# Performance work log

Hardware: AMD Instinct MI355X
Metric: run time of the kernel (lower is better)

The kernel has to match this reference:

```python
import jax, jax.numpy as jnp
import numpy as np

EPS = 1e-5
NUM_HEADS = 8

def _ln(x, g, b):
    mu = jnp.mean(x, axis=-1, keepdims=True)
    var = jnp.mean(jnp.square(x - mu), axis=-1, keepdims=True)
    return (x - mu) * jax.lax.rsqrt(var + EPS) * g + b

def setup_inputs() -> dict:
    key = jax.random.key(0)
    ks = jax.random.split(key, 20)
    B, S, N, D, F = 16, 12, 325, 256, 2048
    sd = 0.02
    return {
        "x": jax.random.normal(ks[0], (B, S, N, D), jnp.float32),
        "Wq": jax.random.normal(ks[1], (D, D), jnp.float32) * sd,
        "bq": jax.random.normal(ks[2], (D,), jnp.float32) * sd,
        "Wk": jax.random.normal(ks[3], (D, D), jnp.float32) * sd,
        "bk": jax.random.normal(ks[4], (D,), jnp.float32) * sd,
        "Wv": jax.random.normal(ks[5], (D, D), jnp.float32) * sd,
        "bv": jax.random.normal(ks[6], (D,), jnp.float32) * sd,
        "Wo": jax.random.normal(ks[7], (D, D), jnp.float32) * sd,
        "bo": jax.random.normal(ks[8], (D,), jnp.float32) * sd,
        "W1": jax.random.normal(ks[9], (D, F), jnp.float32) * sd,
        "b1": jax.random.normal(ks[10], (F,), jnp.float32) * sd,
        "W2": jax.random.normal(ks[11], (F, D), jnp.float32) * sd,
        "b2": jax.random.normal(ks[12], (D,), jnp.float32) * sd,
        "g1": jax.random.uniform(ks[13], (D,), jnp.float32, 0.5, 1.5),
        "beta1": jax.random.normal(ks[14], (D,), jnp.float32) * sd,
        "g2": jax.random.uniform(ks[15], (D,), jnp.float32, 0.5, 1.5),
        "beta2": jax.random.normal(ks[16], (D,), jnp.float32) * sd,
        "dim": -2,
    }

def reference(x, Wq, bq, Wk, bk, Wv, bv, Wo, bo, W1, b1, W2, b2, g1, beta1, g2, beta2, dim):
    # transpose attention dim to -2 (identity when dim == -2)
    x = jnp.swapaxes(x, dim, -2)
    B, S, N, D = x.shape
    H = NUM_HEADS
    hd = D // H
    residual = x
    # QKV projections
    q = (x @ Wq + bq).reshape(B, S, N, H, hd)
    k = (x @ Wk + bk).reshape(B, S, N, H, hd)
    v = (x @ Wv + bv).reshape(B, S, N, H, hd)
    # attention over node dim (axis -2), per head; scale by sqrt(head_dim)
    scores = jnp.einsum('bsnhd,bsmhd->bshnm', q, k) / jnp.sqrt(jnp.float32(hd))
    attn = jax.nn.softmax(scores, axis=-1)
    out = jnp.einsum('bshnm,bsmhd->bsnhd', attn, v).reshape(B, S, N, D)
    out = out @ Wo + bo
    # dropout is identity (p=0); residual + LN
    out = _ln(residual + out, g1, beta1)
    residual = out
    ff = jax.nn.relu(out @ W1 + b1) @ W2 + b2
    out = _ln(residual + ff, g2, beta2)
    return jnp.swapaxes(out, dim, -2)
```

## Files before the change

kernel.cpp:

```cpp
#include <hip/hip_runtime.h>

typedef unsigned short ushortT;
typedef unsigned short us4 __attribute__((ext_vector_type(4)));
typedef short s4 __attribute__((ext_vector_type(4)));
typedef short s8 __attribute__((ext_vector_type(8)));
typedef float f4 __attribute__((ext_vector_type(4)));

__device__ __forceinline__ float bf2f(ushortT u) {
  union { unsigned u; float f; } x; x.u = ((unsigned)u) << 16; return x.f;
}
__device__ __forceinline__ ushortT f2bf(float f) {
  union { float f; unsigned u; } x; x.f = f;
  unsigned r = x.u + 0x7fffu + ((x.u >> 16) & 1u);
  return (ushortT)(r >> 16);
}
__device__ __forceinline__ ushortT bftrunc(float f) {
  union { float f; unsigned u; } x; x.f = f;
  return (ushortT)(x.u >> 16);
}
__device__ __forceinline__ s4 lo4(s8 v) { return __builtin_shufflevector(v, v, 0, 1, 2, 3); }
__device__ __forceinline__ s4 hi4(s8 v) { return __builtin_shufflevector(v, v, 4, 5, 6, 7); }
__device__ __forceinline__ s8 cat(s4 a, s4 b) { return __builtin_shufflevector(a, b, 0, 1, 2, 3, 4, 5, 6, 7); }

__device__ __forceinline__ void gld16(const ushortT* g, ushortT* l) {
  __builtin_amdgcn_global_load_lds(
      (const __attribute__((address_space(1))) void*)g,
      (__attribute__((address_space(3))) void*)l, 16, 0, 0);
}

#define CONV_BLOCKS 15600
__global__ void prep(const float* __restrict__ x,
                     const float* __restrict__ Wq, const float* __restrict__ Wk,
                     const float* __restrict__ Wv, const float* __restrict__ Wo,
                     const float* __restrict__ W1, const float* __restrict__ W2,
                     const float* __restrict__ bq, const float* __restrict__ bk,
                     const float* __restrict__ bv,
                     ushortT* __restrict__ xb, ushortT* __restrict__ WqkvT,
                     ushortT* __restrict__ WoT, ushortT* __restrict__ W1T,
                     ushortT* __restrict__ W2P, float* __restrict__ bqkv)
{
  if (blockIdx.x < CONV_BLOCKS) {
    size_t base = ((size_t)blockIdx.x * 256 + threadIdx.x) * 4;
    f4 v = *(const f4*)(x + base);
    us4 o; o[0]=f2bf(v[0]); o[1]=f2bf(v[1]); o[2]=f2bf(v[2]); o[3]=f2bf(v[3]);
    *(us4*)(xb + base) = o;
    return;
  }
  long e = (long)(blockIdx.x - CONV_BLOCKS) * 256 + threadIdx.x;
  if (e < 196608) {
    int seg = e >> 16; int p = e & 65535; int r = p >> 8, c = p & 255;
    const float* W = seg == 0 ? Wq : (seg == 1 ? Wk : Wv);
    WqkvT[(size_t)(seg * 256 + c) * 256 + r] = f2bf(W[p]);
  } else if (e < 262144) {
    int p = e - 196608; int r = p >> 8, c = p & 255;
    WoT[(size_t)c * 256 + r] = f2bf(Wo[p]);
  } else if (e < 786432) {
    int p = e - 262144; int r = p >> 11, c = p & 2047;
    W1T[(size_t)c * 256 + r] = f2bf(W1[p]);
  } else if (e < 1310720) {
    int p = e - 786432; int r = p >> 8, c = p & 255;
    int rp = (r & ~63) | ((r & 15) << 2) | ((r >> 4) & 3);
    W2P[(size_t)c * 2048 + rp] = f2bf(W2[p]);
  } else {
    int p = (int)(e - 1310720);
    const float* b = (p >> 8) == 0 ? bq : ((p >> 8) == 1 ? bv : bv);
    b = (p >> 8) == 0 ? bq : ((p >> 8) == 1 ? bk : bv);
    bqkv[p] = b[p & 255];
  }
}
#define PREP_BLOCKS (CONV_BLOCKS + 5123)

#define BM 128
#define BN 128
#define BK 32

template <typename CT>
__global__ __launch_bounds__(256, 4) void gemm_async(
    const ushortT* __restrict__ A, const ushortT* __restrict__ Bt,
    const float* __restrict__ bias,
    CT* __restrict__ O0, CT* __restrict__ O1, CT* __restrict__ O2,
    int M, int N, int K, int relu, int route, float s0)
{
  __shared__ ushortT As[BM * BK];
  __shared__ ushortT Bs[BN * BK];
  const int tileN = blockIdx.x * BN;
  const int tileM = blockIdx.y * BM;
  const int tid  = threadIdx.x;
  const int wave = tid >> 6, lane = tid & 63;
  const int wm = (wave >> 1) * 64, wn = (wave & 1) * 64;
  const int lrow = lane & 15;
  const int kq = (lane >> 4) * 8;

  const int srow = wave * 16 + (lane >> 2);
  const int scol = (lane & 3) * 8;
  int ar0 = tileM + srow;        if (ar0 > M - 1) ar0 = M - 1;
  int ar1 = tileM + 64 + srow;   if (ar1 > M - 1) ar1 = M - 1;
  const ushortT* ap0 = A + (size_t)ar0 * K + scol;
  const ushortT* ap1 = A + (size_t)ar1 * K + scol;
  const ushortT* bp0 = Bt + (size_t)(tileN + srow) * K + scol;
  const ushortT* bp1 = Bt + (size_t)(tileN + 64 + srow) * K + scol;
  ushortT* asd0 = As + wave * 512;
  ushortT* asd1 = As + 2048 + wave * 512;
  ushortT* bsd0 = Bs + wave * 512;
  ushortT* bsd1 = Bs + 2048 + wave * 512;

  f4 acc[4][4];
#pragma unroll
  for (int i = 0; i < 4; i++)
#pragma unroll
    for (int j = 0; j < 4; j++) acc[i][j] = 0.f;

  for (int k0 = 0; k0 < K; k0 += BK) {
    gld16(ap0, asd0); gld16(ap1, asd1);
    gld16(bp0, bsd0); gld16(bp1, bsd1);
    ap0 += BK; ap1 += BK; bp0 += BK; bp1 += BK;
    __syncthreads();
    s8 af[4], bfr[4];
#pragma unroll
    for (int mi = 0; mi < 4; mi++)
      af[mi] = *(const s8*)(As + (wm + mi * 16 + lrow) * BK + kq);
#pragma unroll
    for (int ni = 0; ni < 4; ni++)
      bfr[ni] = *(const s8*)(Bs + (wn + ni * 16 + lrow) * BK + kq);
#pragma unroll
    for (int mi = 0; mi < 4; mi++)
#pragma unroll
      for (int ni = 0; ni < 4; ni++)
        acc[mi][ni] = __builtin_amdgcn_mfma_f32_16x16x32_bf16(af[mi], bfr[ni], acc[mi][ni], 0, 0, 0);
    __syncthreads();
  }

  CT* dst; int col0, ostride;
  float oscale = 1.f;
  if (route) {
    int seg = tileN >> 8;
    dst = seg == 0 ? O0 : (seg == 1 ? O1 : O2);
    col0 = tileN & 255; ostride = 256;
    if (seg == 0) oscale = s0;
  } else {
    dst = O0; col0 = tileN; ostride = N;
  }
  const int crow0 = (lane >> 4) * 4;
  const int ccol  = lane & 15;
#pragma unroll
  for (int mi = 0; mi < 4; mi++) {
#pragma unroll
    for (int ni = 0; ni < 4; ni++) {
      int lcol = wn + ni * 16 + ccol;
      float bvv = bias[tileN + lcol];
#pragma unroll
      for (int r = 0; r < 4; r++) {
        int grow = tileM + wm + mi * 16 + crow0 + r;
        if (grow < M) {
          float v = (acc[mi][ni][r] + bvv) * oscale;
          if (relu) v = fmaxf(v, 0.f);
          if constexpr (sizeof(CT) == 2)
            dst[(size_t)grow * ostride + col0 + lcol] = f2bf(v);
          else
            dst[(size_t)grow * ostride + col0 + lcol] = v;
        }
      }
    }
  }
}

#define NQ 325
#define NPAD 384
#define KSTR 36
#define VSTR 388
#define PSTR 72

__global__ __launch_bounds__(256, 2) void attn_mfma(
    const ushortT* __restrict__ q, const ushortT* __restrict__ k,
    const ushortT* __restrict__ v, ushortT* __restrict__ out)
{
  __shared__ ushortT ks[NPAD * KSTR];
  __shared__ ushortT vt[32 * VSTR];
  __shared__ ushortT ps[4 * 16 * PSTR];
  const int bs = blockIdx.x >> 3;
  const int h  = blockIdx.x & 7;
  const size_t rowbase = (size_t)bs * NQ;
  const int hcol = h * 32;
  const int tid = threadIdx.x;
  const int wave = tid >> 6, lane = tid & 63;
  const int g = lane >> 4;
  const int c = lane & 15;

  for (int idx = tid; idx < NPAD * 4; idx += 256) {
    int row = idx >> 2, part = idx & 3;
    s8 kv = 0, vv = 0;
    if (row < NQ) {
      kv = *(const s8*)(k + (rowbase + row) * 256 + hcol + part * 8);
      vv = *(const s8*)(v + (rowbase + row) * 256 + hcol + part * 8);
    }
    *(s4*)(ks + row * KSTR + part * 8)     = lo4(kv);
    *(s4*)(ks + row * KSTR + part * 8 + 4) = hi4(kv);
    int pcol = (row & ~63) | ((row & 15) << 2) | ((row >> 4) & 3);
#pragma unroll
    for (int j = 0; j < 8; j++)
      vt[(part * 8 + j) * VSTR + pcol] = (ushortT)vv[j];
  }
  __syncthreads();

  s8 ones;
#pragma unroll
  for (int j = 0; j < 8; j++) ones[j] = (short)0x3F80;

  ushortT* psw = ps + wave * 16 * PSTR;

  for (int strip = wave; strip < 21; strip += 4) {
    const int m0 = strip * 16;
    s8 qf = 0;
    {
      int qrow = m0 + c;
      if (qrow < NQ) qf = *(const s8*)(q + (rowbase + qrow) * 256 + hcol + g * 8);
    }
    f4 ov0 = 0.f, ov1 = 0.f, ovs = 0.f;

    for (int ch = 0; ch < 6; ++ch) {
      const int nbase = ch * 64;
      f4 sc[4];
#pragma unroll
      for (int t = 0; t < 4; ++t) {
        const ushortT* kr = ks + (nbase + t * 16 + c) * KSTR + g * 8;
        s8 kf = cat(*(const s4*)kr, *(const s4*)(kr + 4));
        f4 z = 0.f;
        sc[t] = __builtin_amdgcn_mfma_f32_16x16x32_bf16(qf, kf, z, 0, 0, 0);
      }
#pragma unroll
      for (int t = 0; t < 4; ++t)
#pragma unroll
        for (int r = 0; r < 4; ++r)
          sc[t][r] = __expf(sc[t][r]);
      if (ch == 5) {
#pragma unroll
        for (int t = 0; t < 4; ++t) {
          bool valid = (t == 0) && (c < 5);
#pragma unroll
          for (int r = 0; r < 4; ++r)
            if (!valid) sc[t][r] = 0.f;
        }
      }
#pragma unroll
      for (int r = 0; r < 4; ++r) {
        us4 pw;
#pragma unroll
        for (int t = 0; t < 4; ++t) pw[t] = bftrunc(sc[t][r]);
        *(us4*)(psw + (g * 4 + r) * PSTR + c * 4) = pw;
      }
#pragma unroll
      for (int kt = 0; kt < 2; ++kt) {
        s8 pf = *(const s8*)(psw + c * PSTR + kt * 32 + g * 8);
        ovs = __builtin_amdgcn_mfma_f32_16x16x32_bf16(pf, ones, ovs, 0, 0, 0);
        const ushortT* vr0 = vt + c * VSTR + nbase + kt * 32 + g * 8;
        const ushortT* vr1 = vt + (16 + c) * VSTR + nbase + kt * 32 + g * 8;
        s8 vf0 = cat(*(const s4*)vr0, *(const s4*)(vr0 + 4));
        s8 vf1 = cat(*(const s4*)vr1, *(const s4*)(vr1 + 4));
        ov0 = __builtin_amdgcn_mfma_f32_16x16x32_bf16(pf, vf0, ov0, 0, 0, 0);
        ov1 = __builtin_amdgcn_mfma_f32_16x16x32_bf16(pf, vf1, ov1, 0, 0, 0);
      }
    }
#pragma unroll
    for (int r = 0; r < 4; ++r) {
      int gm = m0 + g * 4 + r;
      if (gm < NQ) {
        float inv = 1.f / ovs[r];
        out[(rowbase + gm) * 256 + hcol + c]      = f2bf(ov0[r] * inv);
        out[(rowbase + gm) * 256 + hcol + 16 + c] = f2bf(ov1[r] * inv);
      }
    }
  }
}

#define HSTR2 72

__global__ __launch_bounds__(512, 2) void ffn_fused(
    const ushortT* __restrict__ y, const ushortT* __restrict__ W1T,
    const float* __restrict__ b1, const ushortT* __restrict__ W2P,
    const float* __restrict__ b2, float* __restrict__ outp, int M)
{
  __shared__ ushortT w1c[2][64 * 256];
  __shared__ ushortT w2c[2][256 * 64];
  __shared__ ushortT hs[128 * HSTR2];
  __shared__ ushortT b1l[2048];

  const int tid = threadIdx.x;
  const int w = tid >> 6, lane = tid & 63;
  const int g = lane >> 4, c = lane & 15;
  const int mq = w >> 1, nh = w & 1;
  const int Mtile = blockIdx.x * 128;

  {
    f4 bv = *(const f4*)(b1 + tid * 4);
    us4 o; o[0]=f2bf(bv[0]); o[1]=f2bf(bv[1]); o[2]=f2bf(bv[2]); o[3]=f2bf(bv[3]);
    *(us4*)(b1l + tid * 4) = o;
  }

#pragma unroll
  for (int i = 0; i < 4; ++i) {
    int qq = tid * 8 + i * 4096;
    int r1 = qq >> 8;
    int c1 = (qq & 255) ^ ((r1 & 7) << 3);
    gld16(W1T + (size_t)r1 * 256 + c1, w1c[0] + w * 512 + i * 4096);
    int r2 = qq >> 6;
    int c2 = (qq & 63) ^ ((r2 & 7) << 3);
    gld16(W2P + (size_t)r2 * 2048 + c2, w2c[0] + w * 512 + i * 4096);
  }

  int yrow = Mtile + w * 16 + c; if (yrow > M - 1) yrow = M - 1;
  const ushortT* yp = y + (size_t)yrow * 256 + g * 8;
  s8 yv[8];
#pragma unroll
  for (int ksi = 0; ksi < 8; ++ksi) yv[ksi] = *(const s8*)(yp + ksi * 32);

  float b2v[8];
#pragma unroll
  for (int nt = 0; nt < 8; ++nt) b2v[nt] = b2[nh * 128 + nt * 16 + c];

  f4 acc[2][8];
#pragma unroll
  for (int mt = 0; mt < 2; ++mt)
#pragma unroll
    for (int nt = 0; nt < 8; ++nt) acc[mt][nt] = 0.f;

  __syncthreads();

  for (int chn = 0; chn < 32; ++chn) {
    const int b = chn & 1;
    const ushortT* w1b = w1c[b];
    const ushortT* w2b = w2c[b];

    if (chn + 1 < 32) {
      const size_t f1 = (size_t)(chn + 1) * 64 * 256;
      const int k1 = (chn + 1) * 64;
#pragma unroll
      for (int i = 0; i < 4; ++i) {
        int qq = tid * 8 + i * 4096;
        int r1 = qq >> 8;
        int c1 = (qq & 255) ^ ((r1 & 7) << 3);
        gld16(W1T + f1 + (size_t)r1 * 256 + c1, w1c[b ^ 1] + w * 512 + i * 4096);
        int r2 = qq >> 6;
        int c2 = (qq & 63) ^ ((r2 & 7) << 3);
        gld16(W2P + (size_t)r2 * 2048 + k1 + c2, w2c[b ^ 1] + w * 512 + i * 4096);
      }
    }

    f4 sc[4];
#pragma unroll
    for (int t = 0; t < 4; ++t) sc[t] = 0.f;
#pragma unroll
    for (int ksi = 0; ksi < 8; ++ksi) {
#pragma unroll
      for (int t = 0; t < 4; ++t) {
        int f = t * 16 + c;
        s8 wf = *(const s8*)(w1b + f * 256 + ((ksi * 32 + g * 8) ^ ((f & 7) << 3)));
        sc[t] = __builtin_amdgcn_mfma_f32_16x16x32_bf16(yv[ksi], wf, sc[t], 0, 0, 0);
      }
    }
#pragma unroll
    for (int t = 0; t < 4; ++t) {
      float bv = bf2f(b1l[chn * 64 + t * 16 + c]);
#pragma unroll
      for (int r = 0; r < 4; ++r) sc[t][r] = fmaxf(sc[t][r] + bv, 0.f);
    }
#pragma unroll
    for (int r = 0; r < 4; ++r) {
      us4 pw;
#pragma unroll
      for (int t = 0; t < 4; ++t) pw[t] = f2bf(sc[t][r]);
      *(us4*)(hs + (w * 16 + g * 4 + r) * HSTR2 + c * 4) = pw;
    }
    s8 w2a[8];
#pragma unroll
    for (int nt = 0; nt < 8; ++nt) {
      int n = nh * 128 + nt * 16 + c;
      w2a[nt] = *(const s8*)(w2b + n * 64 + ((g * 8) ^ ((n & 7) << 3)));
    }

    asm volatile("s_waitcnt lgkmcnt(0)" ::: "memory");
    __builtin_amdgcn_s_barrier();
    __builtin_amdgcn_sched_barrier(0);

    const ushortT* hrow0 = hs + (mq * 32 + c) * HSTR2;
    const ushortT* hrow1 = hs + (mq * 32 + 16 + c) * HSTR2;
    s8 pf00 = *(const s8*)(hrow0 + g * 8);
    s8 pf10 = *(const s8*)(hrow1 + g * 8);
    s8 pf01 = *(const s8*)(hrow0 + 32 + g * 8);
    s8 pf11 = *(const s8*)(hrow1 + 32 + g * 8);
#pragma unroll
    for (int nt = 0; nt < 8; ++nt) {
      acc[0][nt] = __builtin_amdgcn_mfma_f32_16x16x32_bf16(pf00, w2a[nt], acc[0][nt], 0, 0, 0);
      acc[1][nt] = __builtin_amdgcn_mfma_f32_16x16x32_bf16(pf10, w2a[nt], acc[1][nt], 0, 0, 0);
    }
#pragma unroll
    for (int nt = 0; nt < 8; ++nt) {
      int n = nh * 128 + nt * 16 + c;
      s8 w2f = *(const s8*)(w2b + n * 64 + (((32 + g * 8)) ^ ((n & 7) << 3)));
      acc[0][nt] = __builtin_amdgcn_mfma_f32_16x16x32_bf16(pf01, w2f, acc[0][nt], 0, 0, 0);
      acc[1][nt] = __builtin_amdgcn_mfma_f32_16x16x32_bf16(pf11, w2f, acc[1][nt], 0, 0, 0);
    }

    asm volatile("s_waitcnt vmcnt(0) lgkmcnt(0)" ::: "memory");
    __builtin_amdgcn_s_barrier();
    __builtin_amdgcn_sched_barrier(0);
  }

#pragma unroll
  for (int mt = 0; mt < 2; ++mt) {
#pragma unroll
    for (int r = 0; r < 4; ++r) {
      int grow = Mtile + mq * 32 + mt * 16 + g * 4 + r;
      if (grow < M) {
#pragma unroll
        for (int nt = 0; nt < 8; ++nt)
          outp[(size_t)grow * 256 + nh * 128 + nt * 16 + c] = acc[mt][nt][r] + b2v[nt];
      }
    }
  }
}

template <typename RT, typename VT, typename OT>
__global__ __launch_bounds__(256) void add_ln(
    const RT* __restrict__ res, const VT* __restrict__ val,
    const float* __restrict__ g, const float* __restrict__ beta,
    OT* __restrict__ out, int Mrows)
{
  int row = blockIdx.x * 4 + (threadIdx.x >> 6);
  int lane = threadIdx.x & 63;
  if (row >= Mrows) return;
  float x[4];
  {
    float rvf[4], vvf[4];
    if constexpr (sizeof(RT) == 2) {
      us4 rv = ((const us4*)((const ushortT*)res + (size_t)row * 256))[lane];
      rvf[0]=bf2f(rv[0]); rvf[1]=bf2f(rv[1]); rvf[2]=bf2f(rv[2]); rvf[3]=bf2f(rv[3]);
    } else {
      f4 rv = ((const f4*)((const float*)res + (size_t)row * 256))[lane];
      rvf[0]=rv[0]; rvf[1]=rv[1]; rvf[2]=rv[2]; rvf[3]=rv[3];
    }
    if constexpr (sizeof(VT) == 2) {
      us4 vv = ((const us4*)((const ushortT*)val + (size_t)row * 256))[lane];
      vvf[0]=bf2f(vv[0]); vvf[1]=bf2f(vv[1]); vvf[2]=bf2f(vv[2]); vvf[3]=bf2f(vv[3]);
    } else {
      f4 vv = ((const f4*)((const float*)val + (size_t)row * 256))[lane];
      vvf[0]=vv[0]; vvf[1]=vv[1]; vvf[2]=vv[2]; vvf[3]=vv[3];
    }
#pragma unroll
    for (int j = 0; j < 4; j++) x[j] = rvf[j] + vvf[j];
  }
  float s1 = x[0] + x[1] + x[2] + x[3];
  float s2 = x[0]*x[0] + x[1]*x[1] + x[2]*x[2] + x[3]*x[3];
#pragma unroll
  for (int off = 32; off; off >>= 1) {
    s1 += __shfl_xor(s1, off);
    s2 += __shfl_xor(s2, off);
  }
  float mean = s1 * (1.f / 256.f);
  float var  = s2 * (1.f / 256.f) - mean * mean;
  float rstd = rsqrtf(var + 1e-5f);
  f4 gv = ((const f4*)g)[lane], bv = ((const f4*)beta)[lane];
  if constexpr (sizeof(OT) == 2) {
    us4 o;
#pragma unroll
    for (int j = 0; j < 4; j++)
      o[j] = f2bf((x[j] - mean) * rstd * gv[j] + bv[j]);
    ((us4*)((ushortT*)out + (size_t)row * 256))[lane] = o;
  } else {
    f4 o;
#pragma unroll
    for (int j = 0; j < 4; j++)
      o[j] = (x[j] - mean) * rstd * gv[j] + bv[j];
    ((f4*)((float*)out + (size_t)row * 256))[lane] = o;
  }
}

extern "C" void kernel_launch(void* const* d_in, const int* in_sizes, int n_in,
                              void* d_out, int out_size, void* d_ws, size_t ws_size,
                              hipStream_t stream) {
  const float* x   = (const float*)d_in[0];
  const float* Wq  = (const float*)d_in[1];
  const float* bq  = (const float*)d_in[2];
  const float* Wk  = (const float*)d_in[3];
  const float* bk  = (const float*)d_in[4];
  const float* Wv  = (const float*)d_in[5];
  const float* bv  = (const float*)d_in[6];
  const float* Wo  = (const float*)d_in[7];
  const float* bo  = (const float*)d_in[8];
  const float* W1  = (const float*)d_in[9];
  const float* b1  = (const float*)d_in[10];
  const float* W2  = (const float*)d_in[11];
  const float* b2  = (const float*)d_in[12];
  const float* g1  = (const float*)d_in[13];
  const float* be1 = (const float*)d_in[14];
  const float* g2  = (const float*)d_in[15];
  const float* be2 = (const float*)d_in[16];
  float* outp = (float*)d_out;

  const int M = 16 * 12 * 325;
  const int D = 256;

  ushortT* ws    = (ushortT*)d_ws;
  ushortT* WqkvT = ws;
  ushortT* WoT   = ws + 196608;
  ushortT* W1T   = ws + 262144;
  ushortT* W2P   = ws + 786432;
  float*   bqkv  = (float*)(ws + 1310720);
  ushortT* kb    = ws + 2097152;
  ushortT* vb    = kb + 16777216;
  ushortT* qb = (ushortT*)d_out;
  ushortT* xb = qb + (size_t)M * D;
  ushortT* ob = kb;
  ushortT* y1 = vb;

  dim3 blk(256);

  prep<<<PREP_BLOCKS, blk, 0, stream>>>(x, Wq, Wk, Wv, Wo, W1, W2, bq, bk, bv,
                                        xb, WqkvT, WoT, W1T, W2P, bqkv);

  int mt = (M + BM - 1) / BM;
  const float qscale = 0.17677669529663687f;

  gemm_async<ushortT><<<dim3(768 / BN, mt), blk, 0, stream>>>(
      xb, WqkvT, bqkv, qb, kb, vb, M, 768, D, 0, 1, qscale);

  attn_mfma<<<dim3(192 * 8), blk, 0, stream>>>(qb, kb, vb, qb);

  gemm_async<ushortT><<<dim3(D / BN, mt), blk, 0, stream>>>(
      qb, WoT, bo, ob, ob, ob, M, D, D, 0, 0, 1.f);

  add_ln<float, ushortT, ushortT><<<dim3((M + 3) / 4), blk, 0, stream>>>(x, ob, g1, be1, y1, M);

  ffn_fused<<<dim3((M + 127) / 128), dim3(512), 0, stream>>>(
      y1, W1T, b1, W2P, b2, outp, M);

  add_ln<ushortT, float, float><<<dim3((M + 3) / 4), blk, 0, stream>>>(y1, outp, g2, be2, outp, M);
}
```

Before: 514.8 us.

## Double-buffer GEMM LDS tiles and retile FFN warps for more fragment reuse

The generic GEMM now keeps two LDS buffers and prefetches the next K-tile while computing the current one, waiting with vmcnt instead of a full sync. The bias load moves ahead of the main loop. The fused FFN kernel reassigns waves: each wave computes a 32x32 slice of the hidden chunk over two row tiles, and a 64x64 output tile in the second GEMM. This is meant to raise MFMA-per-LDS-load reuse and cut redundant W2 fragment reads. The cost is more LDS in the GEMM, which can reduce occupancy, plus more accumulator registers.

```diff
diff --git a/kernel.cpp b/kernel.cpp
--- a/kernel.cpp
+++ b/kernel.cpp
@@ -1,6 +1,7 @@
 #include <hip/hip_runtime.h>
 
 typedef unsigned short ushortT;
+typedef unsigned short us2 __attribute__((ext_vector_type(2)));
 typedef unsigned short us4 __attribute__((ext_vector_type(4)));
 typedef short s4 __attribute__((ext_vector_type(4)));
 typedef short s8 __attribute__((ext_vector_type(8)));
@@ -63,8 +64,7 @@
     W2P[(size_t)c * 2048 + rp] = f2bf(W2[p]);
   } else {
     int p = (int)(e - 1310720);
-    const float* b = (p >> 8) == 0 ? bq : ((p >> 8) == 1 ? bv : bv);
-    b = (p >> 8) == 0 ? bq : ((p >> 8) == 1 ? bk : bv);
+    const float* b = (p >> 8) == 0 ? bq : ((p >> 8) == 1 ? bk : bv);
     bqkv[p] = b[p & 255];
   }
 }
@@ -81,8 +81,8 @@
     CT* __restrict__ O0, CT* __restrict__ O1, CT* __restrict__ O2,
     int M, int N, int K, int relu, int route, float s0)
 {
-  __shared__ ushortT As[BM * BK];
-  __shared__ ushortT Bs[BN * BK];
+  __shared__ ushortT As[2][BM * BK];
+  __shared__ ushortT Bs[2][BN * BK];
   const int tileN = blockIdx.x * BN;
   const int tileM = blockIdx.y * BM;
   const int tid  = threadIdx.x;
@@ -90,6 +90,8 @@
   const int wm = (wave >> 1) * 64, wn = (wave & 1) * 64;
   const int lrow = lane & 15;
   const int kq = (lane >> 4) * 8;
+  const int crow0 = (lane >> 4) * 4;
+  const int ccol  = lane & 15;
 
   const int srow = wave * 16 + (lane >> 2);
   const int scol = (lane & 3) * 8;
@@ -99,10 +101,13 @@
   const ushortT* ap1 = A + (size_t)ar1 * K + scol;
   const ushortT* bp0 = Bt + (size_t)(tileN + srow) * K + scol;
   const ushortT* bp1 = Bt + (size_t)(tileN + 64 + srow) * K + scol;
-  ushortT* asd0 = As + wave * 512;
-  ushortT* asd1 = As + 2048 + wave * 512;
-  ushortT* bsd0 = Bs + wave * 512;
-  ushortT* bsd1 = Bs + 2048 + wave * 512;
+  const int d0 = wave * 512;
+  const int d1 = 2048 + wave * 512;
+
+  float bvv[4];
+#pragma unroll
+  for (int ni = 0; ni < 4; ni++) bvv[ni] = bias[tileN + wn + ni * 16 + ccol];
+  asm volatile("" :: "v"(bvv[0]), "v"(bvv[1]), "v"(bvv[2]), "v"(bvv[3]));
 
   f4 acc[4][4];
 #pragma unroll
@@ -110,24 +115,42 @@
 #pragma unroll
     for (int j = 0; j < 4; j++) acc[i][j] = 0.f;
 
-  for (int k0 = 0; k0 < K; k0 += BK) {
-    gld16(ap0, asd0); gld16(ap1, asd1);
-    gld16(bp0, bsd0); gld16(bp1, bsd1);
+  gld16(ap0, As[0] + d0); gld16(ap1, As[0] + d1);
+  gld16(bp0, Bs[0] + d0); gld16(bp1, Bs[0] + d1);
+  ap0 += BK; ap1 += BK; bp0 += BK; bp1 += BK;
+  if (BK < K) {
+    gld16(ap0, As[1] + d0); gld16(ap1, As[1] + d1);
+    gld16(bp0, Bs[1] + d0); gld16(bp1, Bs[1] + d1);
     ap0 += BK; ap1 += BK; bp0 += BK; bp1 += BK;
-    __syncthreads();
+  }
+
+  int cur = 0;
+  for (int k0 = 0; k0 < K; k0 += BK, cur ^= 1) {
+    if (k0 + BK < K) asm volatile("s_waitcnt vmcnt(4)" ::: "memory");
+    else             asm volatile("s_waitcnt vmcnt(0)" ::: "memory");
+    __builtin_amdgcn_s_barrier();
+    __builtin_amdgcn_sched_barrier(0);
+
     s8 af[4], bfr[4];
 #pragma unroll
     for (int mi = 0; mi < 4; mi++)
-      af[mi] = *(const s8*)(As + (wm + mi * 16 + lrow) * BK + kq);
+      af[mi] = *(const s8*)(&As[cur][(wm + mi * 16 + lrow) * BK + kq]);
 #pragma unroll
     for (int ni = 0; ni < 4; ni++)
-      bfr[ni] = *(const s8*)(Bs + (wn + ni * 16 + lrow) * BK + kq);
+      bfr[ni] = *(const s8*)(&Bs[cur][(wn + ni * 16 + lrow) * BK + kq]);
 #pragma unroll
     for (int mi = 0; mi < 4; mi++)
 #pragma unroll
       for (int ni = 0; ni < 4; ni++)
         acc[mi][ni] = __builtin_amdgcn_mfma_f32_16x16x32_bf16(af[mi], bfr[ni], acc[mi][ni], 0, 0, 0);
-    __syncthreads();
+
+    __builtin_amdgcn_s_barrier();
+    __builtin_amdgcn_sched_barrier(0);
+    if (k0 + 2 * BK < K) {
+      gld16(ap0, As[cur] + d0); gld16(ap1, As[cur] + d1);
+      gld16(bp0, Bs[cur] + d0); gld16(bp1, Bs[cur] + d1);
+      ap0 += BK; ap1 += BK; bp0 += BK; bp1 += BK;
+    }
   }
 
   CT* dst; int col0, ostride;
@@ -140,19 +163,16 @@
   } else {
     dst = O0; col0 = tileN; ostride = N;
   }
-  const int crow0 = (lane >> 4) * 4;
-  const int ccol  = lane & 15;
 #pragma unroll
   for (int mi = 0; mi < 4; mi++) {
 #pragma unroll
     for (int ni = 0; ni < 4; ni++) {
       int lcol = wn + ni * 16 + ccol;
-      float bvv = bias[tileN + lcol];
 #pragma unroll
       for (int r = 0; r < 4; r++) {
         int grow = tileM + wm + mi * 16 + crow0 + r;
         if (grow < M) {
-          float v = (acc[mi][ni][r] + bvv) * oscale;
+          float v = (acc[mi][ni][r] + bvv[ni]) * oscale;
           if (relu) v = fmaxf(v, 0.f);
           if constexpr (sizeof(CT) == 2)
             dst[(size_t)grow * ostride + col0 + lcol] = f2bf(v);
@@ -287,7 +307,8 @@
   const int tid = threadIdx.x;
   const int w = tid >> 6, lane = tid & 63;
   const int g = lane >> 4, c = lane & 15;
-  const int mq = w >> 1, nh = w & 1;
+  const int rq = w >> 1, fh = w & 1;
+  const int mq2 = w >> 2, nq = w & 3;
   const int Mtile = blockIdx.x * 128;
 
   {
@@ -307,21 +328,24 @@
     gld16(W2P + (size_t)r2 * 2048 + c2, w2c[0] + w * 512 + i * 4096);
   }
 
-  int yrow = Mtile + w * 16 + c; if (yrow > M - 1) yrow = M - 1;
-  const ushortT* yp = y + (size_t)yrow * 256 + g * 8;
-  s8 yv[8];
-#pragma unroll
-  for (int ksi = 0; ksi < 8; ++ksi) yv[ksi] = *(const s8*)(yp + ksi * 32);
-
-  float b2v[8];
-#pragma unroll
-  for (int nt = 0; nt < 8; ++nt) b2v[nt] = b2[nh * 128 + nt * 16 + c];
-
-  f4 acc[2][8];
-#pragma unroll
-  for (int mt = 0; mt < 2; ++mt)
-#pragma unroll
-    for (int nt = 0; nt < 8; ++nt) acc[mt][nt] = 0.f;
+  s8 yv[2][8];
+#pragma unroll
+  for (int mi = 0; mi < 2; ++mi) {
+    int yrow = Mtile + rq * 32 + mi * 16 + c; if (yrow > M - 1) yrow = M - 1;
+    const ushortT* yp = y + (size_t)yrow * 256 + g * 8;
+#pragma unroll
+    for (int ksi = 0; ksi < 8; ++ksi) yv[mi][ksi] = *(const s8*)(yp + ksi * 32);
+  }
+
+  float b2v[4];
+#pragma unroll
+  for (int ni = 0; ni < 4; ++ni) b2v[ni] = b2[nq * 64 + ni * 16 + c];
+
+  f4 acc[4][4];
+#pragma unroll
+  for (int mi = 0; mi < 4; ++mi)
+#pragma unroll
+    for (int ni = 0; ni < 4; ++ni) acc[mi][ni] = 0.f;
 
   __syncthreads();
 
@@ -345,59 +369,57 @@
       }
     }
 
-    f4 sc[4];
-#pragma unroll
-    for (int t = 0; t < 4; ++t) sc[t] = 0.f;
+    f4 sc[2][2];
+#pragma unroll
+    for (int mi = 0; mi < 2; ++mi)
+#pragma unroll
+      for (int t = 0; t < 2; ++t) sc[mi][t] = 0.f;
 #pragma unroll
     for (int ksi = 0; ksi < 8; ++ksi) {
-#pragma unroll
-      for (int t = 0; t < 4; ++t) {
-        int f = t * 16 + c;
-        s8 wf = *(const s8*)(w1b + f * 256 + ((ksi * 32 + g * 8) ^ ((f & 7) << 3)));
-        sc[t] = __builtin_amdgcn_mfma_f32_16x16x32_bf16(yv[ksi], wf, sc[t], 0, 0, 0);
-      }
-    }
-#pragma unroll
-    for (int t = 0; t < 4; ++t) {
-      float bv = bf2f(b1l[chn * 64 + t * 16 + c]);
-#pragma unroll
-      for (int r = 0; r < 4; ++r) sc[t][r] = fmaxf(sc[t][r] + bv, 0.f);
-    }
-#pragma unroll
-    for (int r = 0; r < 4; ++r) {
-      us4 pw;
-#pragma unroll
-      for (int t = 0; t < 4; ++t) pw[t] = f2bf(sc[t][r]);
-      *(us4*)(hs + (w * 16 + g * 4 + r) * HSTR2 + c * 4) = pw;
-    }
-    s8 w2a[8];
-#pragma unroll
-    for (int nt = 0; nt < 8; ++nt) {
-      int n = nh * 128 + nt * 16 + c;
-      w2a[nt] = *(const s8*)(w2b + n * 64 + ((g * 8) ^ ((n & 7) << 3)));
-    }
+      int f0 = fh * 32 + c;
+      int f1f = fh * 32 + 16 + c;
+      s8 wf0 = *(const s8*)(w1b + f0 * 256 + ((ksi * 32 + g * 8) ^ ((c & 7) << 3)));
+      s8 wf1 = *(const s8*)(w1b + f1f * 256 + ((ksi * 32 + g * 8) ^ ((c & 7) << 3)));
+#pragma unroll
+      for (int mi = 0; mi < 2; ++mi) {
+        sc[mi][0] = __builtin_amdgcn_mfma_f32_16x16x32_bf16(yv[mi][ksi], wf0, sc[mi][0], 0, 0, 0);
+        sc[mi][1] = __builtin_amdgcn_mfma_f32_16x16x32_bf16(yv[mi][ksi], wf1, sc[mi][1], 0, 0, 0);
+      }
+    }
+#pragma unroll
+    for (int t = 0; t < 2; ++t) {
+      float bv = bf2f(b1l[chn * 64 + fh * 32 + t * 16 + c]);
+#pragma unroll
+      for (int mi = 0; mi < 2; ++mi)
+#pragma unroll
+        for (int r = 0; r < 4; ++r) sc[mi][t][r] = fmaxf(sc[mi][t][r] + bv, 0.f);
+    }
+#pragma unroll
+    for (int mi = 0; mi < 2; ++mi)
+#pragma unroll
+      for (int r = 0; r < 4; ++r) {
+        us2 pw; pw[0] = f2bf(sc[mi][0][r]); pw[1] = f2bf(sc[mi][1][r]);
+        *(us2*)(hs + (rq * 32 + mi * 16 + g * 4 + r) * HSTR2 + c * 4 + fh * 2) = pw;
+      }
 
     asm volatile("s_waitcnt lgkmcnt(0)" ::: "memory");
     __builtin_amdgcn_s_barrier();
     __builtin_amdgcn_sched_barrier(0);
 
-    const ushortT* hrow0 = hs + (mq * 32 + c) * HSTR2;
-    const ushortT* hrow1 = hs + (mq * 32 + 16 + c) * HSTR2;
-    s8 pf00 = *(const s8*)(hrow0 + g * 8);
-    s8 pf10 = *(const s8*)(hrow1 + g * 8);
-    s8 pf01 = *(const s8*)(hrow0 + 32 + g * 8);
-    s8 pf11 = *(const s8*)(hrow1 + 32 + g * 8);
-#pragma unroll
-    for (int nt = 0; nt < 8; ++nt) {
-      acc[0][nt] = __builtin_amdgcn_mfma_f32_16x16x32_bf16(pf00, w2a[nt], acc[0][nt], 0, 0, 0);
-      acc[1][nt] = __builtin_amdgcn_mfma_f32_16x16x32_bf16(pf10, w2a[nt], acc[1][nt], 0, 0, 0);
-    }
-#pragma unroll
-    for (int nt = 0; nt < 8; ++nt) {
-      int n = nh * 128 + nt * 16 + c;
-      s8 w2f = *(const s8*)(w2b + n * 64 + (((32 + g * 8)) ^ ((n & 7) << 3)));
-      acc[0][nt] = __builtin_amdgcn_mfma_f32_16x16x32_bf16(pf01, w2f, acc[0][nt], 0, 0, 0);
-      acc[1][nt] = __builtin_amdgcn_mfma_f32_16x16x32_bf16(pf11, w2f, acc[1][nt], 0, 0, 0);
+#pragma unroll
+    for (int kt = 0; kt < 2; ++kt) {
+      s8 pf[4];
+#pragma unroll
+      for (int mi = 0; mi < 4; ++mi)
+        pf[mi] = *(const s8*)(hs + (mq2 * 64 + mi * 16 + c) * HSTR2 + kt * 32 + g * 8);
+#pragma unroll
+      for (int ni = 0; ni < 4; ++ni) {
+        int n = nq * 64 + ni * 16 + c;
+        s8 w2f = *(const s8*)(w2b + n * 64 + ((kt * 32 + g * 8) ^ ((n & 7) << 3)));
+#pragma unroll
+        for (int mi = 0; mi < 4; ++mi)
+          acc[mi][ni] = __builtin_amdgcn_mfma_f32_16x16x32_bf16(pf[mi], w2f, acc[mi][ni], 0, 0, 0);
+      }
     }
 
     asm volatile("s_waitcnt vmcnt(0) lgkmcnt(0)" ::: "memory");
@@ -406,14 +428,14 @@
   }
 
 #pragma unroll
-  for (int mt = 0; mt < 2; ++mt) {
+  for (int mi = 0; mi < 4; ++mi) {
 #pragma unroll
     for (int r = 0; r < 4; ++r) {
-      int grow = Mtile + mq * 32 + mt * 16 + g * 4 + r;
+      int grow = Mtile + mq2 * 64 + mi * 16 + g * 4 + r;
       if (grow < M) {
 #pragma unroll
-        for (int nt = 0; nt < 8; ++nt)
-          outp[(size_t)grow * 256 + nh * 128 + nt * 16 + c] = acc[mt][nt][r] + b2v[nt];
+        for (int ni = 0; ni < 4; ++ni)
+          outp[(size_t)grow * 256 + nq * 64 + ni * 16 + c] = acc[mi][ni][r] + b2v[ni];
       }
     }
   }
```

New measurement: 479.9 us. -6.8%, faster.
